# Optimization experiments

Hardware: AMD Instinct MI355X
Metric: run time of the kernel (lower is better)

## Reference

```python
import jax, jax.numpy as jnp
import numpy as np

EMBED_DIM = 1024
NUM_HEADS = 16
HEAD_DIM = EMBED_DIM // NUM_HEADS


def setup_inputs() -> dict:
    key = jax.random.key(0)
    kx, kq, kk, kv, ko = jax.random.split(key, 5)
    scale = 1.0 / np.sqrt(EMBED_DIM)
    return {
        "x": jax.random.normal(kx, (4, 2048, EMBED_DIM), dtype=jnp.float32),
        # nn.Linear weights are [out, in]; y = x @ W.T
        "w_q": jax.random.normal(kq, (EMBED_DIM, EMBED_DIM), dtype=jnp.float32) * scale,
        "w_k": jax.random.normal(kk, (EMBED_DIM, EMBED_DIM), dtype=jnp.float32) * scale,
        "w_v": jax.random.normal(kv, (EMBED_DIM, EMBED_DIM), dtype=jnp.float32) * scale,
        "w_o": jax.random.normal(ko, (EMBED_DIM, EMBED_DIM), dtype=jnp.float32) * scale,
    }


def reference(x, w_q, w_k, w_v, w_o):
    b, s, _ = x.shape
    # projections (Linear with no bias: x @ W.T)
    q = (x @ w_q.T).reshape(b, s, NUM_HEADS, HEAD_DIM).transpose(0, 2, 1, 3)
    k = (x @ w_k.T).reshape(b, s, NUM_HEADS, HEAD_DIM).transpose(0, 2, 1, 3)
    v = (x @ w_v.T).reshape(b, s, NUM_HEADS, HEAD_DIM).transpose(0, 2, 1, 3)
    # scores: [b, h, s, s]
    scores = jnp.einsum("bhqd,bhkd->bhqk", q, k) / jnp.sqrt(jnp.float32(HEAD_DIM)).astype(x.dtype)
    attn = jax.nn.softmax(scores, axis=-1)
    out = jnp.einsum("bhqk,bhkd->bhqd", attn, v)  # [b, h, s, d]
    out = out.transpose(0, 2, 1, 3).reshape(b, s, EMBED_DIM)
    return out @ w_o.T
```

## Files before the change

### kernel.cpp

```cpp
#include <hip/hip_runtime.h>
#include <math.h>

#define EMBED 1024
#define NHEAD 16
#define HDIM  64
#define BATCH 4
#define SEQ   2048
#define MROWS (BATCH * SEQ)

typedef __attribute__((ext_vector_type(4))) short short4v;
typedef __attribute__((ext_vector_type(8))) short short8;
typedef __attribute__((ext_vector_type(4))) float floatx4;
typedef __attribute__((ext_vector_type(16))) float floatx16;

#if __has_builtin(__builtin_amdgcn_exp2f)
#define EXP2(x) __builtin_amdgcn_exp2f(x)
#else
#define EXP2(x) exp2f(x)
#endif

__device__ __forceinline__ unsigned short f2bf(float f) {
  unsigned u = __float_as_uint(f);
  u += 0x7fffu + ((u >> 16) & 1u);
  return (unsigned short)(u >> 16);
}

#if __has_builtin(__builtin_amdgcn_cvt_pk_bf16_f32)
__device__ __forceinline__ unsigned pack2bf(float lo, float hi) {
  typedef __attribute__((ext_vector_type(2))) __bf16 bf2;
  union { bf2 b; unsigned u; } c;
  c.b = __builtin_amdgcn_cvt_pk_bf16_f32(lo, hi);
  return c.u;
}
#else
__device__ __forceinline__ unsigned pack2bf(float lo, float hi) {
  return ((__float_as_uint(lo) + 0x8000u) >> 16) |
         ((__float_as_uint(hi) + 0x8000u) & 0xffff0000u);
}
#endif

__device__ __forceinline__ void gl_lds16(const void* g, void* l) {
  __builtin_amdgcn_global_load_lds(
      (const __attribute__((address_space(1))) unsigned int*)g,
      (__attribute__((address_space(3))) unsigned int*)l, 16, 0, 0);
}

__global__ __launch_bounds__(256) void cast_bf16_kernel(
    const float* __restrict__ x,  const float* __restrict__ wq,
    const float* __restrict__ wk, const float* __restrict__ wv,
    const float* __restrict__ wo,
    unsigned short* __restrict__ xb, unsigned short* __restrict__ wb) {
  const size_t NX = (size_t)MROWS * EMBED;
  size_t i4 = ((size_t)blockIdx.x * 256 + threadIdx.x) * 4;
  const float* src;
  unsigned short* dst;
  size_t off;
  if (i4 < NX) {
    src = x; dst = xb; off = i4;
  } else {
    size_t j = i4 - NX;
    int r = (int)(j >> 20);
    off = j & ((1u << 20) - 1);
    src = (r == 0) ? wq : (r == 1) ? wk : (r == 2) ? wv : wo;
    dst = wb + ((size_t)r << 20);
  }
  float4 v = *(const float4*)(src + off);
  ushort4 o;
  o.x = f2bf(v.x); o.y = f2bf(v.y); o.z = f2bf(v.z); o.w = f2bf(v.w);
  *(ushort4*)(dst + off) = o;
}

__device__ __forceinline__ void gemm_core(
    const unsigned short* __restrict__ Amat,
    const unsigned short* __restrict__ Bmat,
    int mBase, int nBase,
    unsigned short* As, unsigned short* Bs,
    floatx4 acc[4][4]) {
  const int t = threadIdx.x;
  const int lane = t & 63, w = t >> 6;
  const int wr = w >> 1, wc = w & 1;
  const int quad = lane >> 4, l15 = lane & 15;

  const int f0 = (w * 2 + 0) * 64 + lane;
  const int f1 = (w * 2 + 1) * 64 + lane;
  const unsigned short* ga0 = Amat + (size_t)(mBase + (f0 >> 2)) * EMBED + (f0 & 3) * 8;
  const unsigned short* ga1 = Amat + (size_t)(mBase + (f1 >> 2)) * EMBED + (f1 & 3) * 8;
  const unsigned short* gb0 = Bmat + (size_t)(nBase + (f0 >> 2)) * EMBED + (f0 & 3) * 8;
  const unsigned short* gb1 = Bmat + (size_t)(nBase + (f1 >> 2)) * EMBED + (f1 & 3) * 8;
  unsigned short* la0 = As + (w * 2 + 0) * 512;
  unsigned short* la1 = As + (w * 2 + 1) * 512;
  unsigned short* lb0 = Bs + (w * 2 + 0) * 512;
  unsigned short* lb1 = Bs + (w * 2 + 1) * 512;

  for (int kb = 0; kb < EMBED; kb += 32) {
    __syncthreads();
    gl_lds16(ga0 + kb, la0);
    gl_lds16(ga1 + kb, la1);
    gl_lds16(gb0 + kb, lb0);
    gl_lds16(gb1 + kb, lb1);
    __syncthreads();
    short8 a[4], b[4];
#pragma unroll
    for (int mi = 0; mi < 4; ++mi)
      a[mi] = *(const short8*)&As[(wr * 64 + mi * 16 + l15) * 32 + quad * 8];
#pragma unroll
    for (int ni = 0; ni < 4; ++ni)
      b[ni] = *(const short8*)&Bs[(wc * 64 + ni * 16 + l15) * 32 + quad * 8];
#pragma unroll
    for (int mi = 0; mi < 4; ++mi)
#pragma unroll
      for (int ni = 0; ni < 4; ++ni)
        acc[mi][ni] = __builtin_amdgcn_mfma_f32_16x16x32_bf16(
            a[mi], b[ni], acc[mi][ni], 0, 0, 0);
  }
}

__global__ __launch_bounds__(256) void proj_qkv_bf16(
    const unsigned short* __restrict__ xb,
    const unsigned short* __restrict__ wb,
    unsigned short* __restrict__ qkv) {
  const int which = blockIdx.z;
  const unsigned short* W = wb + ((size_t)which << 20);
  const int nBase = blockIdx.x * 128;
  const int mBase = blockIdx.y * 128;

  __shared__ unsigned short As[128 * 32];
  __shared__ unsigned short Bs[128 * 32];

  floatx4 acc[4][4] = {};
  gemm_core(xb, W, mBase, nBase, As, Bs, acc);

  const int t = threadIdx.x;
  const int lane = t & 63, w = t >> 6;
  const int wr = w >> 1, wc = w & 1;
  const int quad = lane >> 4, l15 = lane & 15;

  unsigned short* out = qkv + (size_t)which * MROWS * EMBED;
  if (which < 2) {
    const float scale = (which == 0) ? 0.18033688f : 1.0f;
#pragma unroll
    for (int mi = 0; mi < 4; ++mi)
#pragma unroll
      for (int ni = 0; ni < 4; ++ni) {
        const int n = nBase + wc * 64 + ni * 16 + l15;
        const int h = n >> 6, d = n & 63;
#pragma unroll
        for (int r = 0; r < 4; ++r) {
          const int m = mBase + wr * 64 + mi * 16 + quad * 4 + r;
          const int b = m >> 11, s = m & (SEQ - 1);
          out[(((size_t)(b * NHEAD + h) * SEQ) + s) * HDIM + d] =
              f2bf(acc[mi][ni][r] * scale);
        }
      }
  } else {
#pragma unroll
    for (int mi = 0; mi < 4; ++mi) {
      const int m0 = mBase + wr * 64 + mi * 16 + quad * 4;
      const int b = m0 >> 11, s0 = m0 & (SEQ - 1);
#pragma unroll
      for (int ni = 0; ni < 4; ++ni) {
        const int n = nBase + wc * 64 + ni * 16 + l15;
        const int h = n >> 6, d = n & 63;
        ushort4 pk;
        pk.x = f2bf(acc[mi][ni][0]); pk.y = f2bf(acc[mi][ni][1]);
        pk.z = f2bf(acc[mi][ni][2]); pk.w = f2bf(acc[mi][ni][3]);
        *(ushort4*)&out[((size_t)(b * NHEAD + h) * HDIM + d) * SEQ + s0] = pk;
      }
    }
  }
}

__global__ __launch_bounds__(512, 4) void attn_mfma(
    const unsigned short* __restrict__ qkv,
    unsigned short* __restrict__ aout) {
  const unsigned short* Q = qkv;
  const unsigned short* K = qkv + (size_t)MROWS * EMBED;
  const unsigned short* V = qkv + 2 * (size_t)MROWS * EMBED;

  const int id = blockIdx.x;
  const int xcd = id & 7, slot = id >> 3;
  const int bh = xcd * 8 + (slot >> 3);
  const int qBase = (slot & 7) * 256;

  __shared__ unsigned short Ks[2 * 128 * 64];
  __shared__ unsigned short Vs[2 * 64 * 128];

  const int t = threadIdx.x;
  const int lane = t & 63, w = t >> 6;
  const int h2 = lane >> 5;
  const int q31 = lane & 31;

  const unsigned short* qrow =
      Q + ((size_t)bh * SEQ + qBase + w * 32 + q31) * HDIM;
  short8 qa[4];
#pragma unroll
  for (int ds = 0; ds < 4; ++ds)
    qa[ds] = *(const short8*)(qrow + ds * 16 + h2 * 8);

  const unsigned short* kbase = K + (size_t)bh * SEQ * HDIM;
  const unsigned short* vbase = V + (size_t)bh * HDIM * SEQ;
  const unsigned short* gk[2];
  const unsigned short* gv[2];
  unsigned short* lk[2];
  unsigned short* lv[2];
#pragma unroll
  for (int i = 0; i < 2; ++i) {
    const int c = i * 512 + t;
    const int krow = c >> 3, kgrp = (c & 7) ^ (krow & 7);
    gk[i] = kbase + (size_t)krow * HDIM + kgrp * 8;
    const int vd = c >> 4, vj = (c & 15) ^ (vd & 15);
    gv[i] = vbase + (size_t)vd * SEQ + vj * 8;
    const int cu = i * 512 + w * 64;
    lk[i] = Ks + cu * 8;
    lv[i] = Vs + cu * 8;
  }

  floatx16 ot0 = {}, ot1 = {};
  float lacc = 0.0f;

#pragma unroll
  for (int i = 0; i < 2; ++i) {
    gl_lds16(gk[i], lk[i]);
    gl_lds16(gv[i], lv[i]);
  }

  for (int kt = 0; kt < SEQ; kt += 128) {
    const int cb = (kt >> 7) & 1;
    const int nb = cb ^ 1;
    const int nxt = (kt + 128) & (SEQ - 1);
    const int sOff = nb * 8192;
#pragma unroll
    for (int i = 0; i < 2; ++i) {
      gl_lds16(gk[i] + (size_t)nxt * HDIM, lk[i] + sOff);
      gl_lds16(gv[i] + nxt, lv[i] + sOff);
    }
    __builtin_amdgcn_sched_barrier(0);
    asm volatile("s_waitcnt vmcnt(4)" ::: "memory");
    __builtin_amdgcn_s_barrier();

    const int kOff = cb * 8192;
    const int vOff = cb * 8192;

#pragma unroll
    for (int sub = 0; sub < 2; ++sub) {
      const int koff = sub * 64;

      floatx16 st0 = {}, st1 = {};
      __builtin_amdgcn_s_setprio(1);
#pragma unroll
      for (int ds = 0; ds < 4; ++ds) {
        const int g = ds * 2 + h2;
        const int k0 = koff + q31;
        short8 ka0 = *(const short8*)&Ks[kOff + k0 * 64 + ((g ^ (q31 & 7)) * 8)];
        st0 = __builtin_amdgcn_mfma_f32_32x32x16_bf16(ka0, qa[ds], st0, 0, 0, 0);
        const int k1 = koff + 32 + q31;
        short8 ka1 = *(const short8*)&Ks[kOff + k1 * 64 + ((g ^ (q31 & 7)) * 8)];
        st1 = __builtin_amdgcn_mfma_f32_32x32x16_bf16(ka1, qa[ds], st1, 0, 0, 0);
      }
      __builtin_amdgcn_s_setprio(0);

      unsigned pk0[8], pk1[8];
#pragma unroll
      for (int i = 0; i < 8; ++i) {
        float a0 = EXP2(st0[2 * i]), b0 = EXP2(st0[2 * i + 1]);
        float a1 = EXP2(st1[2 * i]), b1 = EXP2(st1[2 * i + 1]);
        lacc += (a0 + b0) + (a1 + b1);
        pk0[i] = pack2bf(a0, b0);
        pk1[i] = pack2bf(a1, b1);
      }

      __builtin_amdgcn_s_setprio(1);
#pragma unroll
      for (int s = 0; s < 8; ++s) {
        const unsigned* pk = (s < 4) ? pk0 : pk1;
        const int rg = s & 3;
        union { unsigned u[2]; short4v v; } pb;
        pb.u[0] = pk[2 * rg + 0];
        pb.u[1] = pk[2 * rg + 1];

        const int g = sub * 8 + s;
        const int pos = ((g ^ (q31 & 15)) * 8) + h2 * 4;
        short4v va0 = *(const short4v*)&Vs[vOff + q31 * 128 + pos];
        ot0 = __builtin_amdgcn_mfma_f32_32x32x8bf16_1k(va0, pb.v, ot0, 0, 0, 0);
        short4v va1 = *(const short4v*)&Vs[vOff + (32 + q31) * 128 + pos];
        ot1 = __builtin_amdgcn_mfma_f32_32x32x8bf16_1k(va1, pb.v, ot1, 0, 0, 0);
      }
      __builtin_amdgcn_s_setprio(0);
    }

    __builtin_amdgcn_sched_barrier(0);
    __builtin_amdgcn_s_barrier();
  }
  asm volatile("s_waitcnt vmcnt(0)" ::: "memory");

  const float tot = lacc + __shfl_xor(lacc, 32);
  const float inv = 1.0f / tot;

  const int b = bh >> 4, hh = bh & 15;
  unsigned short* orow =
      aout + ((size_t)b * SEQ + qBase + w * 32 + q31) * EMBED + hh * HDIM;
#pragma unroll
  for (int rg = 0; rg < 4; ++rg) {
    const int d0 = rg * 8 + h2 * 4;
    ushort4 p0, p1;
    p0.x = f2bf(ot0[4 * rg + 0] * inv); p0.y = f2bf(ot0[4 * rg + 1] * inv);
    p0.z = f2bf(ot0[4 * rg + 2] * inv); p0.w = f2bf(ot0[4 * rg + 3] * inv);
    *(ushort4*)(orow + d0) = p0;
    p1.x = f2bf(ot1[4 * rg + 0] * inv); p1.y = f2bf(ot1[4 * rg + 1] * inv);
    p1.z = f2bf(ot1[4 * rg + 2] * inv); p1.w = f2bf(ot1[4 * rg + 3] * inv);
    *(ushort4*)(orow + 32 + d0) = p1;
  }
}

__global__ __launch_bounds__(256) void out_proj_bf16(
    const unsigned short* __restrict__ aout,
    const unsigned short* __restrict__ wb,
    float* __restrict__ Cout) {
  const int nBase = blockIdx.x * 128;
  const int mBase = blockIdx.y * 128;

  __shared__ unsigned short As[128 * 32];
  __shared__ unsigned short Bs[128 * 32];

  floatx4 acc[4][4] = {};
  gemm_core(aout, wb + ((size_t)3 << 20), mBase, nBase, As, Bs, acc);

  const int t = threadIdx.x;
  const int lane = t & 63, w = t >> 6;
  const int wr = w >> 1, wc = w & 1;
  const int quad = lane >> 4, l15 = lane & 15;

#pragma unroll
  for (int mi = 0; mi < 4; ++mi)
#pragma unroll
    for (int ni = 0; ni < 4; ++ni) {
      const int n = nBase + wc * 64 + ni * 16 + l15;
#pragma unroll
      for (int r = 0; r < 4; ++r) {
        const int m = mBase + wr * 64 + mi * 16 + quad * 4 + r;
        Cout[(size_t)m * EMBED + n] = acc[mi][ni][r];
      }
    }
}

extern "C" void kernel_launch(void* const* d_in, const int* in_sizes, int n_in,
                              void* d_out, int out_size, void* d_ws, size_t ws_size,
                              hipStream_t stream) {
  const float* x  = (const float*)d_in[0];
  const float* wq = (const float*)d_in[1];
  const float* wk = (const float*)d_in[2];
  const float* wv = (const float*)d_in[3];
  const float* wo = (const float*)d_in[4];
  float* out = (float*)d_out;

  char* ws = (char*)d_ws;
  unsigned short* xb   = (unsigned short*)(ws);
  unsigned short* wb   = (unsigned short*)(ws + (16u << 20));
  unsigned short* qkv  = (unsigned short*)(ws + (26u << 20));
  unsigned short* aout = (unsigned short*)(ws + (76u << 20));

  cast_bf16_kernel<<<12288, 256, 0, stream>>>(x, wq, wk, wv, wo, xb, wb);
  proj_qkv_bf16<<<dim3(EMBED / 128, MROWS / 128, 3), 256, 0, stream>>>(xb, wb, qkv);
  attn_mfma<<<512, 512, 0, stream>>>(qkv, aout);
  out_proj_bf16<<<dim3(EMBED / 128, MROWS / 128), 256, 0, stream>>>(aout, wb, out);
}
```

Before: 305.7 us.

## Process two 32-row query tiles per wave to reuse K/V LDS fragments

Each wave in the attention kernel now handles 64 query rows, as two 32-row tiles A and B, instead of 32. Each K and V fragment read from LDS therefore feeds two MFMAs, and the grid halves to 256 blocks of 512 query rows each. This is meant to cut LDS read traffic and K/V global loads per query. In exchange it doubles the accumulator and score registers, lowers the occupancy bound from 4 to 2, and with 256 blocks may leave some of the 256 CUs with less latency hiding.

```diff
diff --git a/kernel.cpp b/kernel.cpp
--- a/kernel.cpp
+++ b/kernel.cpp
@@ -170,7 +170,7 @@
   }
 }
 
-__global__ __launch_bounds__(512, 4) void attn_mfma(
+__global__ __launch_bounds__(512, 2) void attn_mfma(
     const unsigned short* __restrict__ qkv,
     unsigned short* __restrict__ aout) {
   const unsigned short* Q = qkv;
@@ -179,8 +179,8 @@
 
   const int id = blockIdx.x;
   const int xcd = id & 7, slot = id >> 3;
-  const int bh = xcd * 8 + (slot >> 3);
-  const int qBase = (slot & 7) * 256;
+  const int bh = xcd * 8 + (slot >> 2);
+  const int qBase = (slot & 3) * 512;
 
   __shared__ unsigned short Ks[2 * 128 * 64];
   __shared__ unsigned short Vs[2 * 64 * 128];
@@ -190,12 +190,15 @@
   const int h2 = lane >> 5;
   const int q31 = lane & 31;
 
-  const unsigned short* qrow =
-      Q + ((size_t)bh * SEQ + qBase + w * 32 + q31) * HDIM;
-  short8 qa[4];
-#pragma unroll
-  for (int ds = 0; ds < 4; ++ds)
-    qa[ds] = *(const short8*)(qrow + ds * 16 + h2 * 8);
+  const unsigned short* qrowA =
+      Q + ((size_t)bh * SEQ + qBase + w * 64 + q31) * HDIM;
+  const unsigned short* qrowB = qrowA + 32 * HDIM;
+  short8 qaA[4], qaB[4];
+#pragma unroll
+  for (int ds = 0; ds < 4; ++ds) {
+    qaA[ds] = *(const short8*)(qrowA + ds * 16 + h2 * 8);
+    qaB[ds] = *(const short8*)(qrowB + ds * 16 + h2 * 8);
+  }
 
   const unsigned short* kbase = K + (size_t)bh * SEQ * HDIM;
   const unsigned short* vbase = V + (size_t)bh * HDIM * SEQ;
@@ -215,8 +218,9 @@
     lv[i] = Vs + cu * 8;
   }
 
-  floatx16 ot0 = {}, ot1 = {};
-  float lacc = 0.0f;
+  floatx16 otA0 = {}, otA1 = {};
+  floatx16 otB0 = {}, otB1 = {};
+  float laccA = 0.0f, laccB = 0.0f;
 
 #pragma unroll
   for (int i = 0; i < 2; ++i) {
@@ -245,45 +249,57 @@
     for (int sub = 0; sub < 2; ++sub) {
       const int koff = sub * 64;
 
-      floatx16 st0 = {}, st1 = {};
+      floatx16 stA0 = {}, stA1 = {}, stB0 = {}, stB1 = {};
       __builtin_amdgcn_s_setprio(1);
 #pragma unroll
       for (int ds = 0; ds < 4; ++ds) {
         const int g = ds * 2 + h2;
         const int k0 = koff + q31;
         short8 ka0 = *(const short8*)&Ks[kOff + k0 * 64 + ((g ^ (q31 & 7)) * 8)];
-        st0 = __builtin_amdgcn_mfma_f32_32x32x16_bf16(ka0, qa[ds], st0, 0, 0, 0);
+        stA0 = __builtin_amdgcn_mfma_f32_32x32x16_bf16(ka0, qaA[ds], stA0, 0, 0, 0);
+        stB0 = __builtin_amdgcn_mfma_f32_32x32x16_bf16(ka0, qaB[ds], stB0, 0, 0, 0);
         const int k1 = koff + 32 + q31;
         short8 ka1 = *(const short8*)&Ks[kOff + k1 * 64 + ((g ^ (q31 & 7)) * 8)];
-        st1 = __builtin_amdgcn_mfma_f32_32x32x16_bf16(ka1, qa[ds], st1, 0, 0, 0);
+        stA1 = __builtin_amdgcn_mfma_f32_32x32x16_bf16(ka1, qaA[ds], stA1, 0, 0, 0);
+        stB1 = __builtin_amdgcn_mfma_f32_32x32x16_bf16(ka1, qaB[ds], stB1, 0, 0, 0);
       }
       __builtin_amdgcn_s_setprio(0);
 
-      unsigned pk0[8], pk1[8];
+      unsigned pkA0[8], pkA1[8], pkB0[8], pkB1[8];
 #pragma unroll
       for (int i = 0; i < 8; ++i) {
-        float a0 = EXP2(st0[2 * i]), b0 = EXP2(st0[2 * i + 1]);
-        float a1 = EXP2(st1[2 * i]), b1 = EXP2(st1[2 * i + 1]);
-        lacc += (a0 + b0) + (a1 + b1);
-        pk0[i] = pack2bf(a0, b0);
-        pk1[i] = pack2bf(a1, b1);
+        float a0 = EXP2(stA0[2 * i]), b0 = EXP2(stA0[2 * i + 1]);
+        float a1 = EXP2(stA1[2 * i]), b1 = EXP2(stA1[2 * i + 1]);
+        laccA += (a0 + b0) + (a1 + b1);
+        pkA0[i] = pack2bf(a0, b0);
+        pkA1[i] = pack2bf(a1, b1);
+        float c0 = EXP2(stB0[2 * i]), d0 = EXP2(stB0[2 * i + 1]);
+        float c1 = EXP2(stB1[2 * i]), d1 = EXP2(stB1[2 * i + 1]);
+        laccB += (c0 + d0) + (c1 + d1);
+        pkB0[i] = pack2bf(c0, d0);
+        pkB1[i] = pack2bf(c1, d1);
       }
 
       __builtin_amdgcn_s_setprio(1);
 #pragma unroll
       for (int s = 0; s < 8; ++s) {
-        const unsigned* pk = (s < 4) ? pk0 : pk1;
+        const unsigned* pkA = (s < 4) ? pkA0 : pkA1;
+        const unsigned* pkB = (s < 4) ? pkB0 : pkB1;
         const int rg = s & 3;
-        union { unsigned u[2]; short4v v; } pb;
-        pb.u[0] = pk[2 * rg + 0];
-        pb.u[1] = pk[2 * rg + 1];
+        union { unsigned u[2]; short4v v; } pbA, pbB;
+        pbA.u[0] = pkA[2 * rg + 0];
+        pbA.u[1] = pkA[2 * rg + 1];
+        pbB.u[0] = pkB[2 * rg + 0];
+        pbB.u[1] = pkB[2 * rg + 1];
 
         const int g = sub * 8 + s;
         const int pos = ((g ^ (q31 & 15)) * 8) + h2 * 4;
         short4v va0 = *(const short4v*)&Vs[vOff + q31 * 128 + pos];
-        ot0 = __builtin_amdgcn_mfma_f32_32x32x8bf16_1k(va0, pb.v, ot0, 0, 0, 0);
+        otA0 = __builtin_amdgcn_mfma_f32_32x32x8bf16_1k(va0, pbA.v, otA0, 0, 0, 0);
+        otB0 = __builtin_amdgcn_mfma_f32_32x32x8bf16_1k(va0, pbB.v, otB0, 0, 0, 0);
         short4v va1 = *(const short4v*)&Vs[vOff + (32 + q31) * 128 + pos];
-        ot1 = __builtin_amdgcn_mfma_f32_32x32x8bf16_1k(va1, pb.v, ot1, 0, 0, 0);
+        otA1 = __builtin_amdgcn_mfma_f32_32x32x8bf16_1k(va1, pbA.v, otA1, 0, 0, 0);
+        otB1 = __builtin_amdgcn_mfma_f32_32x32x8bf16_1k(va1, pbB.v, otB1, 0, 0, 0);
       }
       __builtin_amdgcn_s_setprio(0);
     }
@@ -293,22 +309,32 @@
   }
   asm volatile("s_waitcnt vmcnt(0)" ::: "memory");
 
-  const float tot = lacc + __shfl_xor(lacc, 32);
-  const float inv = 1.0f / tot;
+  const float totA = laccA + __shfl_xor(laccA, 32);
+  const float totB = laccB + __shfl_xor(laccB, 32);
+  const float invA = 1.0f / totA;
+  const float invB = 1.0f / totB;
 
   const int b = bh >> 4, hh = bh & 15;
-  unsigned short* orow =
-      aout + ((size_t)b * SEQ + qBase + w * 32 + q31) * EMBED + hh * HDIM;
+  unsigned short* orowA =
+      aout + ((size_t)b * SEQ + qBase + w * 64 + q31) * EMBED + hh * HDIM;
+  unsigned short* orowB = orowA + (size_t)32 * EMBED;
 #pragma unroll
   for (int rg = 0; rg < 4; ++rg) {
     const int d0 = rg * 8 + h2 * 4;
     ushort4 p0, p1;
-    p0.x = f2bf(ot0[4 * rg + 0] * inv); p0.y = f2bf(ot0[4 * rg + 1] * inv);
-    p0.z = f2bf(ot0[4 * rg + 2] * inv); p0.w = f2bf(ot0[4 * rg + 3] * inv);
-    *(ushort4*)(orow + d0) = p0;
-    p1.x = f2bf(ot1[4 * rg + 0] * inv); p1.y = f2bf(ot1[4 * rg + 1] * inv);
-    p1.z = f2bf(ot1[4 * rg + 2] * inv); p1.w = f2bf(ot1[4 * rg + 3] * inv);
-    *(ushort4*)(orow + 32 + d0) = p1;
+    p0.x = f2bf(otA0[4 * rg + 0] * invA); p0.y = f2bf(otA0[4 * rg + 1] * invA);
+    p0.z = f2bf(otA0[4 * rg + 2] * invA); p0.w = f2bf(otA0[4 * rg + 3] * invA);
+    *(ushort4*)(orowA + d0) = p0;
+    p1.x = f2bf(otA1[4 * rg + 0] * invA); p1.y = f2bf(otA1[4 * rg + 1] * invA);
+    p1.z = f2bf(otA1[4 * rg + 2] * invA); p1.w = f2bf(otA1[4 * rg + 3] * invA);
+    *(ushort4*)(orowA + 32 + d0) = p1;
+    ushort4 p2, p3;
+    p2.x = f2bf(otB0[4 * rg + 0] * invB); p2.y = f2bf(otB0[4 * rg + 1] * invB);
+    p2.z = f2bf(otB0[4 * rg + 2] * invB); p2.w = f2bf(otB0[4 * rg + 3] * invB);
+    *(ushort4*)(orowB + d0) = p2;
+    p3.x = f2bf(otB1[4 * rg + 0] * invB); p3.y = f2bf(otB1[4 * rg + 1] * invB);
+    p3.z = f2bf(otB1[4 * rg + 2] * invB); p3.w = f2bf(otB1[4 * rg + 3] * invB);
+    *(ushort4*)(orowB + 32 + d0) = p3;
   }
 }
 
@@ -361,6 +387,6 @@
 
   cast_bf16_kernel<<<12288, 256, 0, stream>>>(x, wq, wk, wv, wo, xb, wb);
   proj_qkv_bf16<<<dim3(EMBED / 128, MROWS / 128, 3), 256, 0, stream>>>(xb, wb, qkv);
-  attn_mfma<<<512, 512, 0, stream>>>(qkv, aout);
+  attn_mfma<<<256, 512, 0, stream>>>(qkv, aout);
   out_proj_bf16<<<dim3(EMBED / 128, MROWS / 128), 256, 0, stream>>>(aout, wb, out);
 }
```

Result: faster. 286.4 us (-6.3%).
